# Kernel tuning notes

Hardware: AMD Instinct MI355X
Metric: run time of the kernel (lower is better)

## Reference

```python
import jax, jax.numpy as jnp
import numpy as np

EPS = 1e-12  # F.normalize default eps


def setup_inputs() -> dict:
    key = jax.random.key(0)
    ks = jax.random.split(key, 8)
    b, c, h, w = 8, 192, 128, 128
    s = 0.02
    return {
        "x_in": jax.random.normal(ks[0], (b, c, h, w), dtype=jnp.float32),
        "w_split": jax.random.normal(ks[1], (c, c), dtype=jnp.float32) * s,
        "w_q": jax.random.normal(ks[2], (c, c), dtype=jnp.float32) * s,
        "w_k": jax.random.normal(ks[3], (c, c), dtype=jnp.float32) * s,
        "w_v": jax.random.normal(ks[4], (c, c), dtype=jnp.float32) * s,
        "w_proj": jax.random.normal(ks[5], (c, c), dtype=jnp.float32) * s,
        "b_proj": jax.random.normal(ks[6], (c,), dtype=jnp.float32) * s,
        "w_out": jax.random.normal(ks[7], (c, c), dtype=jnp.float32) * s,
    }


def _l2norm(x):
    # F.normalize(p=2, dim=-1): x / max(||x||, eps)
    n = jnp.sqrt(jnp.sum(x * x, axis=-1, keepdims=True))
    return x / jnp.maximum(n, EPS)


def reference(x_in, w_split, w_q, w_k, w_v, w_proj, b_proj, w_out):
    b, c, h, w = x_in.shape
    # conv_split0: 1x1 conv, no bias -> channel matmul
    x = jnp.einsum('oc,bchw->bohw', w_split, x_in)
    # [b,h,w,c] -> [b,hw,c]
    x = x.transpose(0, 2, 3, 1).reshape(b, h * w, c)
    # Linear: y = x @ W^T
    q = jnp.einsum('bnc,oc->bon', x, w_q)  # [b,c,hw] (already transposed)
    k = jnp.einsum('bnc,oc->bon', x, w_k)
    v = jnp.einsum('bnc,oc->bon', x, w_v)
    q = _l2norm(q)
    k = _l2norm(k)
    attn = jax.nn.softmax(jnp.einsum('bcn,bdn->bcd', k, q), axis=-1)  # [b,c,c]
    y = jnp.einsum('bcd,bdn->bcn', attn, v)  # [b,c,hw]
    y = y.transpose(0, 2, 1)  # [b,hw,c]
    out = jnp.einsum('bnc,oc->bno', y, w_proj) + b_proj
    out = out.reshape(b, h, w, c).transpose(0, 3, 1, 2)  # [b,c,h,w]
    out = jnp.einsum('oc,bchw->bohw', w_out, out)
    return out
```

## Files before the change

### kernel.cpp

```cpp
#include <hip/hip_runtime.h>


static constexpr int B_ = 8;
static constexpr int C_ = 192;
static constexpr int N_ = 16384;
static constexpr int CC2 = C_ * C_;
static constexpr int NCHUNK = 32;

using u16x8 = __attribute__((ext_vector_type(8))) unsigned short;
using bf16x8 = __attribute__((ext_vector_type(8))) __bf16;
using f32x4 = __attribute__((ext_vector_type(4))) float;

__device__ __forceinline__ unsigned short f2bf(float f) {
  unsigned int u = __builtin_bit_cast(unsigned int, f);
  u += 0x7FFFu + ((u >> 16) & 1u);
  return (unsigned short)(u >> 16);
}

__device__ __forceinline__ f32x4 mfma16(u16x8 a, u16x8 b, f32x4 c) {
  return __builtin_amdgcn_mfma_f32_16x16x32_bf16(
      __builtin_bit_cast(bf16x8, a), __builtin_bit_cast(bf16x8, b), c, 0, 0, 0);
}

__global__ void fold_kernel(const float* __restrict__ wsplit, const float* __restrict__ wq,
                            const float* __restrict__ wk, const float* __restrict__ wv,
                            const float* __restrict__ wproj, const float* __restrict__ bproj,
                            const float* __restrict__ wout,
                            float* __restrict__ Wq, float* __restrict__ WqT,
                            float* __restrict__ Wk, float* __restrict__ Wv,
                            float* __restrict__ Wo2, float* __restrict__ bias2) {
  int idx = blockIdx.x * 256 + threadIdx.x;
  if (idx < C_) {
    float s = 0.f;
    for (int c = 0; c < C_; ++c) s += wout[idx * C_ + c] * bproj[c];
    bias2[idx] = s;
  }
  if (idx >= 4 * CC2) return;
  int which = idx / CC2;
  int rem = idx % CC2;
  int o = rem / C_, c = rem % C_;
  const float* A = (which == 0) ? wq : (which == 1) ? wk : (which == 2) ? wv : wout;
  const float* Bm = (which == 3) ? wproj : wsplit;
  float s = 0.f;
  for (int e = 0; e < C_; ++e) s += A[o * C_ + e] * Bm[e * C_ + c];
  if (which == 0) { Wq[rem] = s; WqT[c * C_ + o] = s; }
  else if (which == 1) Wk[rem] = s;
  else if (which == 2) Wv[rem] = s;
  else Wo2[rem] = s;
}

template <bool ATOMIC>
__global__ __launch_bounds__(384) void gram2_kernel(const float* __restrict__ xin,
                                                    float* __restrict__ dst) {
  const int b = blockIdx.y, ch = blockIdx.x;
  const int k0 = ch * 512;
  __shared__ unsigned short Xs[2][C_][72];
  const int tid = threadIdx.x;
  const int wv = tid >> 6;
  const int lane = tid & 63;
  const int ln = lane & 15, mq = lane >> 4;
  const int cbase = tid >> 4;
  const int k4 = tid & 15;
  const float* xb = xin + (size_t)b * C_ * N_;

  f32x4 acc[2][12];
#pragma unroll
  for (int i = 0; i < 2; ++i)
#pragma unroll
    for (int j = 0; j < 12; ++j) acc[i][j] = (f32x4)0.0f;

  float4 ld[8];
  auto load_stage = [&](int kbase) {
#pragma unroll
    for (int j = 0; j < 8; ++j)
      ld[j] = *(const float4*)(xb + (size_t)(j * 24 + cbase) * N_ + kbase + k4 * 4);
  };
  auto write_stage = [&](int buf) {
#pragma unroll
    for (int j = 0; j < 8; ++j) {
      unsigned int lo = (unsigned)f2bf(ld[j].x) | ((unsigned)f2bf(ld[j].y) << 16);
      unsigned int hi = (unsigned)f2bf(ld[j].z) | ((unsigned)f2bf(ld[j].w) << 16);
      uint2 pk; pk.x = lo; pk.y = hi;
      *(uint2*)&Xs[buf][j * 24 + cbase][k4 * 4] = pk;
    }
  };

  load_stage(k0);
  write_stage(0);
  __syncthreads();
  for (int s = 0; s < 8; ++s) {
    if (s < 7) load_stage(k0 + (s + 1) * 64);
    const int cb = s & 1;
#pragma unroll
    for (int ks = 0; ks < 2; ++ks) {
      const int kk = ks * 32 + mq * 8;
      u16x8 a0 = *(const u16x8*)&Xs[cb][32 * wv + ln][kk];
      u16x8 a1 = *(const u16x8*)&Xs[cb][32 * wv + 16 + ln][kk];
#pragma unroll
      for (int ct = 0; ct < 12; ++ct) {
        u16x8 bf = *(const u16x8*)&Xs[cb][ct * 16 + ln][kk];
        acc[0][ct] = mfma16(a0, bf, acc[0][ct]);
        acc[1][ct] = mfma16(a1, bf, acc[1][ct]);
      }
    }
    if (s < 7) {
      write_stage(cb ^ 1);
      __syncthreads();
    }
  }
  float* out = ATOMIC ? dst + (size_t)b * CC2
                      : dst + ((size_t)b * NCHUNK + ch) * CC2;
#pragma unroll
  for (int i = 0; i < 2; ++i)
#pragma unroll
    for (int ct = 0; ct < 12; ++ct)
#pragma unroll
      for (int r = 0; r < 4; ++r) {
        int row = 32 * wv + 16 * i + mq * 4 + r;
        int col = ct * 16 + ln;
        if (ATOMIC) atomicAdd(&out[row * C_ + col], acc[i][ct][r]);
        else out[row * C_ + col] = acc[i][ct][r];
      }
}

__global__ void gsum_kernel(const float* __restrict__ P, float* __restrict__ G) {
  const int j = blockIdx.x * 256 + threadIdx.x;
  const int b = blockIdx.y;
  const float* base = P + (size_t)b * NCHUNK * CC2 + j;
  float s0 = 0.f, s1 = 0.f, s2 = 0.f, s3 = 0.f;
#pragma unroll
  for (int ch = 0; ch < NCHUNK; ch += 4) {
    s0 += base[(size_t)ch * CC2];
    s1 += base[(size_t)(ch + 1) * CC2];
    s2 += base[(size_t)(ch + 2) * CC2];
    s3 += base[(size_t)(ch + 3) * CC2];
  }
  G[(size_t)b * CC2 + j] = (s0 + s1) + (s2 + s3);
}

__global__ void tk_kernel(const float* __restrict__ Wk, const float* __restrict__ G,
                          float* __restrict__ Tk) {
  int idx = blockIdx.x * 256 + threadIdx.x;
  if (idx >= B_ * CC2) return;
  int b = idx / CC2;
  int rc = idx % CC2;
  int d = rc / C_, cp = rc % C_;
  const float* Gb = G + (size_t)b * CC2;
  float s = 0.f;
  for (int c = 0; c < C_; ++c) s += Wk[d * C_ + c] * Gb[c * C_ + cp];
  Tk[idx] = s;
}

__global__ __launch_bounds__(192) void qn_kernel(const float* __restrict__ Wq,
                                                 const float* __restrict__ G,
                                                 float* __restrict__ qn) {
  const int b = blockIdx.y, d = blockIdx.x, t = threadIdx.x;
  const float* Gb = G + (size_t)b * CC2;
  float inner = 0.f;
  for (int c = 0; c < C_; ++c) inner += Wq[d * C_ + c] * Gb[c * C_ + t];
  float val = inner * Wq[d * C_ + t];
  __shared__ float red[256];
  red[t] = val;
  if (t < 64) red[192 + t] = 0.f;
  __syncthreads();
  for (int st = 128; st > 0; st >>= 1) {
    if (t < st) red[t] += red[t + st];
    __syncthreads();
  }
  if (t == 0) qn[b * C_ + d] = fmaxf(sqrtf(fmaxf(red[0], 0.f)), 1e-12f);
}

__global__ __launch_bounds__(192) void attn_av_kernel(const float* __restrict__ Tk,
                                                      const float* __restrict__ WqT,
                                                      const float* __restrict__ Wk,
                                                      const float* __restrict__ Wv,
                                                      const float* __restrict__ qn,
                                                      float* __restrict__ Tv) {
  const int b = blockIdx.y, cc = blockIdx.x, t = threadIdx.x;
  __shared__ float tkrow[C_];
  __shared__ float arow[C_];
  __shared__ float red[256];
  tkrow[t] = Tk[((size_t)b * C_ + cc) * C_ + t];
  red[t] = tkrow[t] * Wk[cc * C_ + t];
  if (t < 64) red[192 + t] = 0.f;
  __syncthreads();
  for (int st = 128; st > 0; st >>= 1) {
    if (t < st) red[t] += red[t + st];
    __syncthreads();
  }
  float knv = fmaxf(sqrtf(fmaxf(red[0], 0.f)), 1e-12f);
  __syncthreads();
  float s = 0.f;
  for (int c = 0; c < C_; ++c) s += tkrow[c] * WqT[c * C_ + t];
  float lg = s / (knv * qn[b * C_ + t]);
  red[t] = lg;
  if (t < 64) red[192 + t] = -1e30f;
  __syncthreads();
  for (int st = 128; st > 0; st >>= 1) {
    if (t < st) red[t] = fmaxf(red[t], red[t + st]);
    __syncthreads();
  }
  float mx = red[0];
  __syncthreads();
  float e = expf(lg - mx);
  red[t] = e;
  if (t < 64) red[192 + t] = 0.f;
  __syncthreads();
  for (int st = 128; st > 0; st >>= 1) {
    if (t < st) red[t] += red[t + st];
    __syncthreads();
  }
  float a = e / red[0];
  arow[t] = a;
  __syncthreads();
  float sv = 0.f;
  for (int c = 0; c < C_; ++c) sv += arow[c] * Wv[c * C_ + t];
  Tv[((size_t)b * C_ + cc) * C_ + t] = sv;
}

__global__ void m_kernel(const float* __restrict__ Wo2, const float* __restrict__ Tv,
                         float* __restrict__ Mout) {
  int idx = blockIdx.x * 256 + threadIdx.x;
  if (idx >= B_ * CC2) return;
  int b = idx / CC2;
  int rc = idx % CC2;
  int i = rc / C_, j = rc % C_;
  float s = 0.f;
  for (int c = 0; c < C_; ++c) s += Wo2[i * C_ + c] * Tv[((size_t)b * C_ + c) * C_ + j];
  Mout[idx] = s;
}

__global__ __launch_bounds__(384) void final_kernel(const float* __restrict__ xin,
                                                    const float* __restrict__ Mw,
                                                    const float* __restrict__ bias2,
                                                    float* __restrict__ out) {
  const int b = blockIdx.y;
  const int p0 = blockIdx.x * 128;
  __shared__ unsigned short Ts[128][200];
  const int tid = threadIdx.x;
  const int wv = tid >> 6;
  const int lane = tid & 63;
  const int ln = lane & 15, mq = lane >> 4;
  const float* Mb = Mw + (size_t)b * CC2;

  u16x8 afr[6][2];
  float bo[2][4];
#pragma unroll
  for (int i = 0; i < 2; ++i) {
    int row = 32 * wv + 16 * i + ln;
#pragma unroll
    for (int kc = 0; kc < 6; ++kc) {
      const float* src = Mb + row * C_ + kc * 32 + mq * 8;
      float4 u0 = *(const float4*)(src);
      float4 u1 = *(const float4*)(src + 4);
      u16x8 a;
      a[0] = f2bf(u0.x); a[1] = f2bf(u0.y); a[2] = f2bf(u0.z); a[3] = f2bf(u0.w);
      a[4] = f2bf(u1.x); a[5] = f2bf(u1.y); a[6] = f2bf(u1.z); a[7] = f2bf(u1.w);
      afr[kc][i] = a;
    }
#pragma unroll
    for (int r = 0; r < 4; ++r) bo[i][r] = bias2[32 * wv + 16 * i + mq * 4 + r];
  }

#pragma unroll
  for (int j = 0; j < 16; ++j) {
    int lin = j * 384 + tid;
    int c = lin >> 5, p4 = lin & 31;
    float4 v = *(const float4*)(xin + ((size_t)b * C_ + c) * N_ + p0 + p4 * 4);
    Ts[p4 * 4 + 0][c] = f2bf(v.x);
    Ts[p4 * 4 + 1][c] = f2bf(v.y);
    Ts[p4 * 4 + 2][c] = f2bf(v.z);
    Ts[p4 * 4 + 3][c] = f2bf(v.w);
  }
  __syncthreads();

#pragma unroll
  for (int pt = 0; pt < 8; ++pt) {
    f32x4 acc0 = (f32x4)0.0f, acc1 = (f32x4)0.0f;
#pragma unroll
    for (int kc = 0; kc < 6; ++kc) {
      u16x8 bf = *(const u16x8*)&Ts[pt * 16 + ln][kc * 32 + mq * 8];
      acc0 = mfma16(afr[kc][0], bf, acc0);
      acc1 = mfma16(afr[kc][1], bf, acc1);
    }
#pragma unroll
    for (int r = 0; r < 4; ++r) {
      int row0 = 32 * wv + mq * 4 + r;
      int row1 = row0 + 16;
      int p = p0 + pt * 16 + ln;
      out[((size_t)b * C_ + row0) * N_ + p] = acc0[r] + bo[0][r];
      out[((size_t)b * C_ + row1) * N_ + p] = acc1[r] + bo[1][r];
    }
  }
}

extern "C" void kernel_launch(void* const* d_in, const int* in_sizes, int n_in,
                              void* d_out, int out_size, void* d_ws, size_t ws_size,
                              hipStream_t stream) {
  const float* xin    = (const float*)d_in[0];
  const float* wsplit = (const float*)d_in[1];
  const float* wq     = (const float*)d_in[2];
  const float* wk     = (const float*)d_in[3];
  const float* wv     = (const float*)d_in[4];
  const float* wvv    = (const float*)d_in[4];
  (void)wvv;
  const float* wproj  = (const float*)d_in[5];
  const float* bproj  = (const float*)d_in[6];
  const float* wout   = (const float*)d_in[7];
  float* out = (float*)d_out;

  float* ws = (float*)d_ws;
  float* G     = ws;
  float* Wq    = G + (size_t)B_ * CC2;
  float* WqT   = Wq + CC2;
  float* Wk    = WqT + CC2;
  float* Wv    = Wk + CC2;
  float* Wo2   = Wv + CC2;
  float* bias2 = Wo2 + CC2;
  float* Tk    = bias2 + 256;
  float* Tv    = Tk + (size_t)B_ * CC2;
  float* Mw    = Tv + (size_t)B_ * CC2;
  float* qn    = Mw + (size_t)B_ * CC2;
  float* P     = qn + 256 * B_;

  size_t base_floats = (size_t)(P - ws);
  size_t need_bytes = (base_floats + (size_t)B_ * NCHUNK * CC2) * sizeof(float);
  bool use_partials = ws_size >= need_bytes;

  fold_kernel<<<(4 * CC2 + 255) / 256, 256, 0, stream>>>(
      wsplit, wq, wk, wv, wproj, bproj, wout, Wq, WqT, Wk, Wv, Wo2, bias2);
  if (use_partials) {
    gram2_kernel<false><<<dim3(NCHUNK, B_), 384, 0, stream>>>(xin, P);
    gsum_kernel<<<dim3(CC2 / 256, B_), 256, 0, stream>>>(P, G);
  } else {
    hipMemsetAsync(G, 0, (size_t)B_ * CC2 * sizeof(float), stream);
    gram2_kernel<true><<<dim3(NCHUNK, B_), 384, 0, stream>>>(xin, G);
  }
  tk_kernel<<<(B_ * CC2 + 255) / 256, 256, 0, stream>>>(Wk, G, Tk);
  qn_kernel<<<dim3(C_, B_), 192, 0, stream>>>(Wq, G, qn);
  attn_av_kernel<<<dim3(C_, B_), 192, 0, stream>>>(Tk, WqT, Wk, Wv, qn, Tv);
  m_kernel<<<(B_ * CC2 + 255) / 256, 256, 0, stream>>>(Wo2, Tv, Mw);
  final_kernel<<<dim3(N_ / 128, B_), 384, 0, stream>>>(xin, Mw, bias2, out);
}
```

Before: 334.7 us.

## Split gram rows across blocks, fuse Tk/qn, vectorize gsum, swizzle final LDS

The Gram kernel now splits its 192 output rows across two blocks per chunk, doubling the grid to raise occupancy, though each block reloads the full X tile. The partial-sum reduction loads float4 vectors, and the Tk and q-norm kernels are merged so G is read once for both. The final kernel replaces its padded transpose buffer with an XOR-swizzled layout to avoid LDS bank conflicts on the scattered bf16 stores.

Result: faster. 323.7 us (-3.3%).

```diff
diff --git a/kernel.cpp b/kernel.cpp
--- a/kernel.cpp
+++ b/kernel.cpp
@@ -50,24 +50,23 @@
 }
 
 template <bool ATOMIC>
-__global__ __launch_bounds__(384) void gram2_kernel(const float* __restrict__ xin,
+__global__ __launch_bounds__(384) void gram3_kernel(const float* __restrict__ xin,
                                                     float* __restrict__ dst) {
-  const int b = blockIdx.y, ch = blockIdx.x;
+  const int b = blockIdx.z, half = blockIdx.y, ch = blockIdx.x;
   const int k0 = ch * 512;
   __shared__ unsigned short Xs[2][C_][72];
   const int tid = threadIdx.x;
   const int wv = tid >> 6;
   const int lane = tid & 63;
   const int ln = lane & 15, mq = lane >> 4;
+  const int arow0 = half * 96 + wv * 16;
   const int cbase = tid >> 4;
   const int k4 = tid & 15;
   const float* xb = xin + (size_t)b * C_ * N_;
 
-  f32x4 acc[2][12];
-#pragma unroll
-  for (int i = 0; i < 2; ++i)
-#pragma unroll
-    for (int j = 0; j < 12; ++j) acc[i][j] = (f32x4)0.0f;
+  f32x4 acc[12];
+#pragma unroll
+  for (int j = 0; j < 12; ++j) acc[j] = (f32x4)0.0f;
 
   float4 ld[8];
   auto load_stage = [&](int kbase) {
@@ -94,13 +93,11 @@
 #pragma unroll
     for (int ks = 0; ks < 2; ++ks) {
       const int kk = ks * 32 + mq * 8;
-      u16x8 a0 = *(const u16x8*)&Xs[cb][32 * wv + ln][kk];
-      u16x8 a1 = *(const u16x8*)&Xs[cb][32 * wv + 16 + ln][kk];
+      u16x8 a0 = *(const u16x8*)&Xs[cb][arow0 + ln][kk];
 #pragma unroll
       for (int ct = 0; ct < 12; ++ct) {
         u16x8 bf = *(const u16x8*)&Xs[cb][ct * 16 + ln][kk];
-        acc[0][ct] = mfma16(a0, bf, acc[0][ct]);
-        acc[1][ct] = mfma16(a1, bf, acc[1][ct]);
+        acc[ct] = mfma16(a0, bf, acc[ct]);
       }
     }
     if (s < 7) {
@@ -111,54 +108,44 @@
   float* out = ATOMIC ? dst + (size_t)b * CC2
                       : dst + ((size_t)b * NCHUNK + ch) * CC2;
 #pragma unroll
-  for (int i = 0; i < 2; ++i)
-#pragma unroll
-    for (int ct = 0; ct < 12; ++ct)
-#pragma unroll
-      for (int r = 0; r < 4; ++r) {
-        int row = 32 * wv + 16 * i + mq * 4 + r;
-        int col = ct * 16 + ln;
-        if (ATOMIC) atomicAdd(&out[row * C_ + col], acc[i][ct][r]);
-        else out[row * C_ + col] = acc[i][ct][r];
-      }
+  for (int ct = 0; ct < 12; ++ct)
+#pragma unroll
+    for (int r = 0; r < 4; ++r) {
+      int row = arow0 + mq * 4 + r;
+      int col = ct * 16 + ln;
+      if (ATOMIC) atomicAdd(&out[row * C_ + col], acc[ct][r]);
+      else out[row * C_ + col] = acc[ct][r];
+    }
 }
 
 __global__ void gsum_kernel(const float* __restrict__ P, float* __restrict__ G) {
-  const int j = blockIdx.x * 256 + threadIdx.x;
+  const int j = (blockIdx.x * 256 + threadIdx.x) * 4;
   const int b = blockIdx.y;
   const float* base = P + (size_t)b * NCHUNK * CC2 + j;
-  float s0 = 0.f, s1 = 0.f, s2 = 0.f, s3 = 0.f;
-#pragma unroll
-  for (int ch = 0; ch < NCHUNK; ch += 4) {
-    s0 += base[(size_t)ch * CC2];
-    s1 += base[(size_t)(ch + 1) * CC2];
-    s2 += base[(size_t)(ch + 2) * CC2];
-    s3 += base[(size_t)(ch + 3) * CC2];
-  }
-  G[(size_t)b * CC2 + j] = (s0 + s1) + (s2 + s3);
-}
-
-__global__ void tk_kernel(const float* __restrict__ Wk, const float* __restrict__ G,
-                          float* __restrict__ Tk) {
-  int idx = blockIdx.x * 256 + threadIdx.x;
-  if (idx >= B_ * CC2) return;
-  int b = idx / CC2;
-  int rc = idx % CC2;
-  int d = rc / C_, cp = rc % C_;
-  const float* Gb = G + (size_t)b * CC2;
-  float s = 0.f;
-  for (int c = 0; c < C_; ++c) s += Wk[d * C_ + c] * Gb[c * C_ + cp];
-  Tk[idx] = s;
-}
-
-__global__ __launch_bounds__(192) void qn_kernel(const float* __restrict__ Wq,
-                                                 const float* __restrict__ G,
-                                                 float* __restrict__ qn) {
+  float4 s = {0.f, 0.f, 0.f, 0.f};
+#pragma unroll
+  for (int ch = 0; ch < NCHUNK; ++ch) {
+    float4 v = *(const float4*)(base + (size_t)ch * CC2);
+    s.x += v.x; s.y += v.y; s.z += v.z; s.w += v.w;
+  }
+  *(float4*)(G + (size_t)b * CC2 + j) = s;
+}
+
+__global__ __launch_bounds__(192) void tkqn_kernel(const float* __restrict__ Wk,
+                                                   const float* __restrict__ Wq,
+                                                   const float* __restrict__ G,
+                                                   float* __restrict__ Tk,
+                                                   float* __restrict__ qn) {
   const int b = blockIdx.y, d = blockIdx.x, t = threadIdx.x;
   const float* Gb = G + (size_t)b * CC2;
-  float inner = 0.f;
-  for (int c = 0; c < C_; ++c) inner += Wq[d * C_ + c] * Gb[c * C_ + t];
-  float val = inner * Wq[d * C_ + t];
+  float sk = 0.f, sq = 0.f;
+  for (int c = 0; c < C_; ++c) {
+    float g = Gb[c * C_ + t];
+    sk += Wk[d * C_ + c] * g;
+    sq += Wq[d * C_ + c] * g;
+  }
+  Tk[((size_t)b * C_ + d) * C_ + t] = sk;
+  float val = sq * Wq[d * C_ + t];
   __shared__ float red[256];
   red[t] = val;
   if (t < 64) red[192 + t] = 0.f;
@@ -230,13 +217,13 @@
   Mout[idx] = s;
 }
 
-__global__ __launch_bounds__(384) void final_kernel(const float* __restrict__ xin,
-                                                    const float* __restrict__ Mw,
-                                                    const float* __restrict__ bias2,
-                                                    float* __restrict__ out) {
+__global__ __launch_bounds__(384) void final2_kernel(const float* __restrict__ xin,
+                                                     const float* __restrict__ Mw,
+                                                     const float* __restrict__ bias2,
+                                                     float* __restrict__ out) {
   const int b = blockIdx.y;
   const int p0 = blockIdx.x * 128;
-  __shared__ unsigned short Ts[128][200];
+  __shared__ unsigned short Ts[128 * 192];
   const int tid = threadIdx.x;
   const int wv = tid >> 6;
   const int lane = tid & 63;
@@ -267,19 +254,24 @@
     int lin = j * 384 + tid;
     int c = lin >> 5, p4 = lin & 31;
     float4 v = *(const float4*)(xin + ((size_t)b * C_ + c) * N_ + p0 + p4 * 4);
-    Ts[p4 * 4 + 0][c] = f2bf(v.x);
-    Ts[p4 * 4 + 1][c] = f2bf(v.y);
-    Ts[p4 * 4 + 2][c] = f2bf(v.z);
-    Ts[p4 * 4 + 3][c] = f2bf(v.w);
+#pragma unroll
+    for (int jj = 0; jj < 4; ++jj) {
+      int e = (jj + (p4 >> 1)) & 3;
+      float val = (e == 0) ? v.x : (e == 1) ? v.y : (e == 2) ? v.z : v.w;
+      int p = p4 * 4 + e;
+      int idx = p * 192 + ((((c >> 3) ^ (p & 7)) << 3) | (c & 7));
+      Ts[idx] = f2bf(val);
+    }
   }
   __syncthreads();
 
 #pragma unroll
   for (int pt = 0; pt < 8; ++pt) {
+    const int p = pt * 16 + ln;
     f32x4 acc0 = (f32x4)0.0f, acc1 = (f32x4)0.0f;
 #pragma unroll
     for (int kc = 0; kc < 6; ++kc) {
-      u16x8 bf = *(const u16x8*)&Ts[pt * 16 + ln][kc * 32 + mq * 8];
+      u16x8 bf = *(const u16x8*)&Ts[p * 192 + (((kc * 4 + mq) ^ (p & 7)) << 3)];
       acc0 = mfma16(afr[kc][0], bf, acc0);
       acc1 = mfma16(afr[kc][1], bf, acc1);
     }
@@ -287,9 +279,9 @@
     for (int r = 0; r < 4; ++r) {
       int row0 = 32 * wv + mq * 4 + r;
       int row1 = row0 + 16;
-      int p = p0 + pt * 16 + ln;
-      out[((size_t)b * C_ + row0) * N_ + p] = acc0[r] + bo[0][r];
-      out[((size_t)b * C_ + row1) * N_ + p] = acc1[r] + bo[1][r];
+      int pp = p0 + pt * 16 + ln;
+      out[((size_t)b * C_ + row0) * N_ + pp] = acc0[r] + bo[0][r];
+      out[((size_t)b * C_ + row1) * N_ + pp] = acc1[r] + bo[1][r];
     }
   }
 }
@@ -302,8 +294,6 @@
   const float* wq     = (const float*)d_in[2];
   const float* wk     = (const float*)d_in[3];
   const float* wv     = (const float*)d_in[4];
-  const float* wvv    = (const float*)d_in[4];
-  (void)wvv;
   const float* wproj  = (const float*)d_in[5];
   const float* bproj  = (const float*)d_in[6];
   const float* wout   = (const float*)d_in[7];
@@ -330,15 +320,14 @@
   fold_kernel<<<(4 * CC2 + 255) / 256, 256, 0, stream>>>(
       wsplit, wq, wk, wv, wproj, bproj, wout, Wq, WqT, Wk, Wv, Wo2, bias2);
   if (use_partials) {
-    gram2_kernel<false><<<dim3(NCHUNK, B_), 384, 0, stream>>>(xin, P);
-    gsum_kernel<<<dim3(CC2 / 256, B_), 256, 0, stream>>>(P, G);
+    gram3_kernel<false><<<dim3(NCHUNK, 2, B_), 384, 0, stream>>>(xin, P);
+    gsum_kernel<<<dim3(CC2 / 1024, B_), 256, 0, stream>>>(P, G);
   } else {
     hipMemsetAsync(G, 0, (size_t)B_ * CC2 * sizeof(float), stream);
-    gram2_kernel<true><<<dim3(NCHUNK, B_), 384, 0, stream>>>(xin, G);
-  }
-  tk_kernel<<<(B_ * CC2 + 255) / 256, 256, 0, stream>>>(Wk, G, Tk);
-  qn_kernel<<<dim3(C_, B_), 192, 0, stream>>>(Wq, G, qn);
+    gram3_kernel<true><<<dim3(NCHUNK, 2, B_), 384, 0, stream>>>(xin, G);
+  }
+  tkqn_kernel<<<dim3(C_, B_), 192, 0, stream>>>(Wk, Wq, G, Tk, qn);
   attn_av_kernel<<<dim3(C_, B_), 192, 0, stream>>>(Tk, WqT, Wk, Wv, qn, Tv);
   m_kernel<<<(B_ * CC2 + 255) / 256, 256, 0, stream>>>(Wo2, Tv, Mw);
-  final_kernel<<<dim3(N_ / 128, B_), 384, 0, stream>>>(xin, Mw, bias2, out);
-}
+  final2_kernel<<<dim3(N_ / 128, B_), 384, 0, stream>>>(xin, Mw, bias2, out);
+}
```
